# Kernel tuning notes

Hardware: AMD Instinct MI355X
Metric: run time of the kernel (lower is better)

## Reference

```python
import jax, jax.numpy as jnp
import numpy as np

N = 50000        # nodes
E = 800000       # edges (avg degree 16)
IN = 256         # in_feature_dim
H = 4            # heads_num
F = 64           # out_feature_dim per head (H*F == IN)
NEG_SLOPE = 0.2  # LeakyReLU slope used for both scoring and output activation


def setup_inputs() -> dict:
    key = jax.random.key(0)
    ks = jax.random.split(key, 8)
    x = jax.random.normal(ks[0], (N, IN), dtype=jnp.float32)
    edge_src = jax.random.randint(ks[1], (E,), 0, N, dtype=jnp.int32)
    edge_trg = jax.random.randint(ks[2], (E,), 0, N, dtype=jnp.int32)
    # xavier-ish scaled params
    W = jax.random.normal(ks[3], (IN, H * F), dtype=jnp.float32) * 0.06
    a_src = jax.random.normal(ks[4], (H, F), dtype=jnp.float32) * 0.1
    a_trg = jax.random.normal(ks[5], (H, F), dtype=jnp.float32) * 0.1
    skip_w = jax.random.normal(ks[6], (IN, H * F), dtype=jnp.float32) * 0.06
    bias = jnp.zeros((H * F,), dtype=jnp.float32)
    return {"x": x, "W": W, "a_src": a_src, "a_trg": a_trg,
            "skip_w": skip_w, "bias": bias,
            "edge_src": edge_src, "edge_trg": edge_trg}


def _leaky(v):
    return jnp.where(v > 0, v, NEG_SLOPE * v)


def reference(x, W, a_src, a_trg, skip_w, bias, edge_src, edge_trg):
    n_nodes = x.shape[0]
    # node-wise projection: [N, H, F]
    proj = (x @ W).reshape(n_nodes, H, F)
    # per-head attention scores: [N, H]
    s_src = jnp.einsum('nhf,hf->nh', proj, a_src)
    s_trg = jnp.einsum('nhf,hf->nh', proj, a_trg)
    # lift to edges + LeakyReLU scoring: [E, H]
    e = _leaky(s_src[edge_src] + s_trg[edge_trg])
    # neighborhood-aware (scatter) softmax over incoming edges of each target
    e = e - jnp.max(e)                      # global max subtraction, as in the source
    ex = jnp.exp(e)
    denom = jax.ops.segment_sum(ex, edge_trg, num_segments=n_nodes)  # [N, H]
    attn = ex / (denom[edge_trg] + 1e-16)   # [E, H]
    # weighted aggregation: [E, H, F] -> scatter-add -> [N, H, F]
    weighted = proj[edge_src] * attn[..., None]
    out = jax.ops.segment_sum(weighted, edge_trg, num_segments=n_nodes)
    # skip connection (dims differ: in=256 vs per-head 64 -> use skip_proj)
    out = out + (x @ skip_w).reshape(n_nodes, H, F)
    # concat heads + bias + output activation (default LeakyReLU 0.2)
    out = out.reshape(n_nodes, H * F) + bias
    return _leaky(out)
```

## Files before the change

### kernel.cpp

```cpp
#include <hip/hip_runtime.h>
#include <math.h>

constexpr float SLOPE = 0.2f;

typedef __bf16 bf16x8 __attribute__((ext_vector_type(8)));
typedef __bf16 bf16x4 __attribute__((ext_vector_type(4)));
typedef float  f32x4  __attribute__((ext_vector_type(4)));

__device__ __forceinline__ int imin(int a, int b) { return a < b ? a : b; }

__device__ __forceinline__ void glds16(const void* g, void* l) {
    __builtin_amdgcn_global_load_lds(
        (const __attribute__((address_space(1))) unsigned int*)g,
        (__attribute__((address_space(3))) unsigned int*)l,
        16, 0, 0);
}

__global__ __launch_bounds__(256) void prep_k(
    const float* __restrict__ W, const float* __restrict__ skw,
    __bf16* __restrict__ Bt,
    const float* __restrict__ x, __bf16* __restrict__ xb, int nxv, int nxb,
    const int* __restrict__ etrg, int* __restrict__ cnt, int E)
{
    const int b = blockIdx.x;
    if (b < 512) {
        const int i = b * 256 + threadIdx.x;
        const int n = i >> 8, k = i & 255;
        const float v = (n < 256) ? W[k * 256 + n] : skw[k * 256 + (n - 256)];
        Bt[i] = (__bf16)v;
    } else if (b < 512 + nxb) {
        const int gid = (b - 512) * 256 + threadIdx.x;
        if (gid < nxv) {
            const float4 f0 = *(const float4*)(x + (size_t)gid * 8);
            const float4 f1 = *(const float4*)(x + (size_t)gid * 8 + 4);
            bf16x8 v;
            v[0] = (__bf16)f0.x; v[1] = (__bf16)f0.y;
            v[2] = (__bf16)f0.z; v[3] = (__bf16)f0.w;
            v[4] = (__bf16)f1.x; v[5] = (__bf16)f1.y;
            v[6] = (__bf16)f1.z; v[7] = (__bf16)f1.w;
            *(bf16x8*)(xb + (size_t)gid * 8) = v;
        }
    } else {
        const int e = (b - 512 - nxb) * 256 + threadIdx.x;
        if (e < E) atomicAdd(&cnt[etrg[e]], 1);
    }
}

__global__ __launch_bounds__(256) void gemm_mfma(
    const __bf16* __restrict__ xb, const __bf16* __restrict__ Bt,
    __bf16* __restrict__ projb, float* __restrict__ out, int M)
{
    __shared__ __bf16 As[128 * 32];
    __shared__ __bf16 Bs[128 * 32];

    const int t    = threadIdx.x;
    const int w    = t >> 6;
    const int lane = t & 63;
    const int q    = lane >> 4;
    const int ln   = lane & 15;

    const int row0 = blockIdx.x * 128;
    const int bt0  = blockIdx.y * 128;

    f32x4 acc[2][8] = {};

    for (int k0 = 0; k0 < 256; k0 += 32) {
#pragma unroll
        for (int p = 0; p < 2; ++p) {
            const int idx = p * 256 + t;
            const int r   = idx >> 2;
            const int ko  = (idx & 3) * 8;
            const int ga  = imin(row0 + r, M - 1);
            glds16(xb + (size_t)ga * 256 + k0 + ko, &As[idx * 8]);
            glds16(Bt + (size_t)(bt0 + r) * 256 + k0 + ko, &Bs[idx * 8]);
        }
        asm volatile("s_waitcnt vmcnt(0)" ::: "memory");
        __syncthreads();

        bf16x8 af[2], bfr[8];
#pragma unroll
        for (int rb = 0; rb < 2; ++rb)
            af[rb] = *(const bf16x8*)&As[(w * 32 + rb * 16 + ln) * 32 + q * 8];
#pragma unroll
        for (int cb = 0; cb < 8; ++cb)
            bfr[cb] = *(const bf16x8*)&Bs[(cb * 16 + ln) * 32 + q * 8];
#pragma unroll
        for (int rb = 0; rb < 2; ++rb)
#pragma unroll
            for (int cb = 0; cb < 8; ++cb)
                acc[rb][cb] = __builtin_amdgcn_mfma_f32_16x16x32_bf16(
                    af[rb], bfr[cb], acc[rb][cb], 0, 0, 0);
        __syncthreads();
    }

    const bool isProj  = (blockIdx.y < 2);
    const int  colbase = (blockIdx.y & 1) * 128;
#pragma unroll
    for (int rb = 0; rb < 2; ++rb) {
#pragma unroll
        for (int r = 0; r < 4; ++r) {
            const int grow = row0 + w * 32 + rb * 16 + q * 4 + r;
            if (grow < M) {
#pragma unroll
                for (int cb = 0; cb < 8; ++cb) {
                    const float v = acc[rb][cb][r];
                    const int gcol = colbase + cb * 16 + ln;
                    if (isProj) projb[(size_t)grow * 256 + gcol] = (__bf16)v;
                    else        out[(size_t)grow * 256 + gcol]   = v;
                }
            }
        }
    }
}

__global__ __launch_bounds__(256) void scores_k(
    const __bf16* __restrict__ projb,
    const float* __restrict__ a_src, const float* __restrict__ a_trg,
    float* __restrict__ s_src, float* __restrict__ s_trg, int N)
{
    const int nid  = blockIdx.x * 4 + (threadIdx.x >> 6);
    const int lane = threadIdx.x & 63;
    if (nid >= N) return;

    const bf16x4 p4  = *(const bf16x4*)(projb + (size_t)nid * 256 + lane * 4);
    const float4 as4 = *(const float4*)(a_src + lane * 4);
    const float4 at4 = *(const float4*)(a_trg + lane * 4);

    float vs = (float)p4[0] * as4.x + (float)p4[1] * as4.y +
               (float)p4[2] * as4.z + (float)p4[3] * as4.w;
    float vt = (float)p4[0] * at4.x + (float)p4[1] * at4.y +
               (float)p4[2] * at4.z + (float)p4[3] * at4.w;

#pragma unroll
    for (int d = 8; d > 0; d >>= 1) {
        vs += __shfl_down(vs, d, 16);
        vt += __shfl_down(vt, d, 16);
    }
    if ((lane & 15) == 0) {
        s_src[nid * 4 + (lane >> 4)] = vs;
        s_trg[nid * 4 + (lane >> 4)] = vt;
    }
}

__global__ __launch_bounds__(1024) void scanA(
    const int* __restrict__ cnt, int* __restrict__ off, int* __restrict__ bsum, int N)
{
    __shared__ int wsum[16];
    const int t = threadIdx.x;
    const int lane = t & 63;
    const int w = t >> 6;
    const int i = blockIdx.x * 1024 + t;
    const int v = (i < N) ? cnt[i] : 0;

    int s = v;
#pragma unroll
    for (int d = 1; d < 64; d <<= 1) {
        int o = __shfl_up(s, d);
        if (lane >= d) s += o;
    }
    if (lane == 63) wsum[w] = s;
    __syncthreads();
    if (w == 0 && lane < 16) {
        int ws = wsum[lane];
        int sc = ws;
#pragma unroll
        for (int d = 1; d < 16; d <<= 1) {
            int o = __shfl_up(sc, d);
            if (lane >= d) sc += o;
        }
        wsum[lane] = sc - ws;
    }
    __syncthreads();
    const int excl = wsum[w] + s - v;
    if (i < N) off[i] = excl;
    if (t == 1023) bsum[blockIdx.x] = excl + v;
}

__global__ __launch_bounds__(256) void scanBC(
    int* __restrict__ off, const int* __restrict__ bsum, int* __restrict__ cur,
    int N, int E)
{
    const int i = blockIdx.x * 256 + threadIdx.x;
    const int chunk = blockIdx.x >> 2;
    const int lane = threadIdx.x & 63;

    int v = (lane < chunk) ? bsum[lane] : 0;
#pragma unroll
    for (int d = 1; d < 64; d <<= 1) v += __shfl_xor(v, d);

    if (i < N) {
        const int o = off[i] + v;
        off[i] = o;
        cur[i] = o;
    }
    if (i == 0) off[N] = E;
}

__global__ __launch_bounds__(256) void scatter_k(
    const int* __restrict__ esrc, const int* __restrict__ etrg,
    int* __restrict__ cur,
    const float* __restrict__ s_src, const float* __restrict__ s_trg,
    int* __restrict__ srcs, float* __restrict__ exs, int E)
{
    const int e = blockIdx.x * 256 + threadIdx.x;
    if (e >= E) return;
    const int s  = esrc[e];
    const int tg = etrg[e];
    const int pos = atomicAdd(&cur[tg], 1);
    srcs[pos] = s;
    const float4 ss = *(const float4*)(s_src + (size_t)s * 4);
    const float4 st = *(const float4*)(s_trg + (size_t)tg * 4);
    float4 ex; float v;
    v = ss.x + st.x; v = v > 0.f ? v : SLOPE * v; ex.x = __expf(v);
    v = ss.y + st.y; v = v > 0.f ? v : SLOPE * v; ex.y = __expf(v);
    v = ss.z + st.z; v = v > 0.f ? v : SLOPE * v; ex.z = __expf(v);
    v = ss.w + st.w; v = v > 0.f ? v : SLOPE * v; ex.w = __expf(v);
    *(float4*)(exs + (size_t)pos * 4) = ex;
}

__global__ __launch_bounds__(256) void aggregate_csr(
    const int* __restrict__ off, const int* __restrict__ srcs,
    const float* __restrict__ exs, const __bf16* __restrict__ projb,
    const float* __restrict__ bias, float* __restrict__ out)
{
    const int n = blockIdx.x;
    const int t = threadIdx.x;
    const int h = t >> 6;

    const int b0 = off[n], b1 = off[n + 1];

    float acc = 0.f, denom = 0.f;
    int i = b0;
    for (; i + 8 <= b1; i += 8) {
        int s[8];
#pragma unroll
        for (int j = 0; j < 8; ++j) s[j] = srcs[i + j];
        float p[8];
#pragma unroll
        for (int j = 0; j < 8; ++j)
            p[j] = (float)projb[(unsigned)s[j] * 256u + t];
        const float* ep = exs + (size_t)i * 4 + h;
        float e[8];
#pragma unroll
        for (int j = 0; j < 8; ++j) e[j] = ep[j * 4];
#pragma unroll
        for (int j = 0; j < 8; ++j) { denom += e[j]; acc += e[j] * p[j]; }
    }
    for (; i < b1; ++i) {
        const int s = srcs[i];
        const float e = exs[(size_t)i * 4 + h];
        denom += e;
        acc += e * (float)projb[(unsigned)s * 256u + t];
    }

    const size_t o = (size_t)n * 256 + t;
    float val = acc / (denom + 1e-16f) + out[o] + bias[t];
    out[o] = val > 0.f ? val : SLOPE * val;
}

extern "C" void kernel_launch(void* const* d_in, const int* in_sizes, int n_in,
                              void* d_out, int out_size, void* d_ws, size_t ws_size,
                              hipStream_t stream)
{
    const float* x     = (const float*)d_in[0];
    const float* W     = (const float*)d_in[1];
    const float* a_src = (const float*)d_in[2];
    const float* a_trg = (const float*)d_in[3];
    const float* skw   = (const float*)d_in[4];
    const float* bias  = (const float*)d_in[5];
    const int*   esrc  = (const int*)d_in[6];
    const int*   etrg  = (const int*)d_in[7];

    const int N = in_sizes[0] / 256;
    const int E = in_sizes[6];
    float* out = (float*)d_out;

    __bf16* projb = (__bf16*)d_ws;
    __bf16* Bt    = projb + (size_t)N * 256;
    __bf16* xb    = Bt + 512 * 256;
    float*  exs   = (float*)xb;
    float*  s_src = (float*)(xb + (size_t)N * 256);
    float*  s_trg = s_src + (size_t)N * 4;
    int*    cnt   = (int*)(s_trg + (size_t)N * 4);
    int*    off   = cnt + N;
    int*    cur   = off + (N + 1);
    int*    bsum  = cur + N;
    int*    srcs  = bsum + 64;

    const int nxv = (N * 256) / 8;
    const int nxb = (nxv + 255) / 256;
    const int nhb = (E + 255) / 256;
    const int nsc = (N + 1023) / 1024;

    hipMemsetAsync(cnt, 0, (size_t)N * sizeof(int), stream);

    prep_k<<<512 + nxb + nhb, 256, 0, stream>>>(W, skw, Bt, x, xb, nxv, nxb,
                                                etrg, cnt, E);

    dim3 g((N + 127) / 128, 4);
    gemm_mfma<<<g, 256, 0, stream>>>(xb, Bt, projb, out, N);

    scores_k<<<(N + 3) / 4, 256, 0, stream>>>(projb, a_src, a_trg, s_src, s_trg, N);

    scanA<<<nsc, 1024, 0, stream>>>(cnt, off, bsum, N);
    scanBC<<<(N + 255) / 256, 256, 0, stream>>>(off, bsum, cur, N, E);

    scatter_k<<<(E + 255) / 256, 256, 0, stream>>>(esrc, etrg, cur, s_src, s_trg,
                                                   srcs, exs, E);

    aggregate_csr<<<N, 256, 0, stream>>>(off, srcs, exs, projb, bias, out);
}
```

Before: 340.6 us.

## Fuse edge scoring into wave-per-node aggregation and enlarge GEMM row tile

Edge score computation (LeakyReLU plus exp) moves from the scatter kernel into a new aggregation kernel. That kernel assigns one 64-lane wave per target node, with each lane handling 4 features via bf16x4 loads, and lanes share source indices and exp values through shuffles. This drops the exs write/read round trip and raises per-lane work in aggregation. Separately, the GEMM tile grows to 256 rows with a launch_bounds occupancy hint, which raises register pressure and lowers block count.

```diff
diff --git a/kernel.cpp b/kernel.cpp
--- a/kernel.cpp
+++ b/kernel.cpp
@@ -46,11 +46,11 @@
     }
 }
 
-__global__ __launch_bounds__(256) void gemm_mfma(
+__global__ __launch_bounds__(256, 2) void gemm_mfma(
     const __bf16* __restrict__ xb, const __bf16* __restrict__ Bt,
     __bf16* __restrict__ projb, float* __restrict__ out, int M)
 {
-    __shared__ __bf16 As[128 * 32];
+    __shared__ __bf16 As[256 * 32];
     __shared__ __bf16 Bs[128 * 32];
 
     const int t    = threadIdx.x;
@@ -59,33 +59,39 @@
     const int q    = lane >> 4;
     const int ln   = lane & 15;
 
-    const int row0 = blockIdx.x * 128;
+    const int row0 = blockIdx.x * 256;
     const int bt0  = blockIdx.y * 128;
 
-    f32x4 acc[2][8] = {};
+    f32x4 acc[4][8] = {};
 
     for (int k0 = 0; k0 < 256; k0 += 32) {
 #pragma unroll
-        for (int p = 0; p < 2; ++p) {
+        for (int p = 0; p < 4; ++p) {
             const int idx = p * 256 + t;
             const int r   = idx >> 2;
             const int ko  = (idx & 3) * 8;
             const int ga  = imin(row0 + r, M - 1);
             glds16(xb + (size_t)ga * 256 + k0 + ko, &As[idx * 8]);
+        }
+#pragma unroll
+        for (int p = 0; p < 2; ++p) {
+            const int idx = p * 256 + t;
+            const int r   = idx >> 2;
+            const int ko  = (idx & 3) * 8;
             glds16(Bt + (size_t)(bt0 + r) * 256 + k0 + ko, &Bs[idx * 8]);
         }
         asm volatile("s_waitcnt vmcnt(0)" ::: "memory");
         __syncthreads();
 
-        bf16x8 af[2], bfr[8];
-#pragma unroll
-        for (int rb = 0; rb < 2; ++rb)
-            af[rb] = *(const bf16x8*)&As[(w * 32 + rb * 16 + ln) * 32 + q * 8];
+        bf16x8 af[4], bfr[8];
+#pragma unroll
+        for (int rb = 0; rb < 4; ++rb)
+            af[rb] = *(const bf16x8*)&As[(w * 64 + rb * 16 + ln) * 32 + q * 8];
 #pragma unroll
         for (int cb = 0; cb < 8; ++cb)
             bfr[cb] = *(const bf16x8*)&Bs[(cb * 16 + ln) * 32 + q * 8];
 #pragma unroll
-        for (int rb = 0; rb < 2; ++rb)
+        for (int rb = 0; rb < 4; ++rb)
 #pragma unroll
             for (int cb = 0; cb < 8; ++cb)
                 acc[rb][cb] = __builtin_amdgcn_mfma_f32_16x16x32_bf16(
@@ -96,10 +102,10 @@
     const bool isProj  = (blockIdx.y < 2);
     const int  colbase = (blockIdx.y & 1) * 128;
 #pragma unroll
-    for (int rb = 0; rb < 2; ++rb) {
+    for (int rb = 0; rb < 4; ++rb) {
 #pragma unroll
         for (int r = 0; r < 4; ++r) {
-            const int grow = row0 + w * 32 + rb * 16 + q * 4 + r;
+            const int grow = row0 + w * 64 + rb * 16 + q * 4 + r;
             if (grow < M) {
 #pragma unroll
                 for (int cb = 0; cb < 8; ++cb) {
@@ -198,64 +204,90 @@
 
 __global__ __launch_bounds__(256) void scatter_k(
     const int* __restrict__ esrc, const int* __restrict__ etrg,
-    int* __restrict__ cur,
+    int* __restrict__ cur, int* __restrict__ srcs, int E)
+{
+    const int e = blockIdx.x * 256 + threadIdx.x;
+    if (e < E) {
+        const int pos = atomicAdd(&cur[etrg[e]], 1);
+        srcs[pos] = esrc[e];
+    }
+}
+
+__global__ __launch_bounds__(256) void aggregate_wave(
+    const int* __restrict__ off, const int* __restrict__ srcs,
     const float* __restrict__ s_src, const float* __restrict__ s_trg,
-    int* __restrict__ srcs, float* __restrict__ exs, int E)
-{
-    const int e = blockIdx.x * 256 + threadIdx.x;
-    if (e >= E) return;
-    const int s  = esrc[e];
-    const int tg = etrg[e];
-    const int pos = atomicAdd(&cur[tg], 1);
-    srcs[pos] = s;
-    const float4 ss = *(const float4*)(s_src + (size_t)s * 4);
-    const float4 st = *(const float4*)(s_trg + (size_t)tg * 4);
-    float4 ex; float v;
-    v = ss.x + st.x; v = v > 0.f ? v : SLOPE * v; ex.x = __expf(v);
-    v = ss.y + st.y; v = v > 0.f ? v : SLOPE * v; ex.y = __expf(v);
-    v = ss.z + st.z; v = v > 0.f ? v : SLOPE * v; ex.z = __expf(v);
-    v = ss.w + st.w; v = v > 0.f ? v : SLOPE * v; ex.w = __expf(v);
-    *(float4*)(exs + (size_t)pos * 4) = ex;
-}
-
-__global__ __launch_bounds__(256) void aggregate_csr(
-    const int* __restrict__ off, const int* __restrict__ srcs,
-    const float* __restrict__ exs, const __bf16* __restrict__ projb,
-    const float* __restrict__ bias, float* __restrict__ out)
-{
-    const int n = blockIdx.x;
-    const int t = threadIdx.x;
-    const int h = t >> 6;
-
+    const __bf16* __restrict__ projb, const float* __restrict__ bias,
+    float* __restrict__ out, int N)
+{
+    const int w = threadIdx.x >> 6;
+    const int l = threadIdx.x & 63;
+    const int n = blockIdx.x * 4 + w;
+    if (n >= N) return;
+
+    const int h  = l >> 4;
+    const int je = l & 7;
+    const float st = s_trg[n * 4 + h];
     const int b0 = off[n], b1 = off[n + 1];
 
-    float acc = 0.f, denom = 0.f;
+    f32x4 acc = {0.f, 0.f, 0.f, 0.f};
+    float denom = 0.f;
+
     int i = b0;
     for (; i + 8 <= b1; i += 8) {
+        const int s0 = srcs[i + je];
+        float v = s_src[s0 * 4 + h] + st;
+        v = v > 0.f ? v : SLOPE * v;
+        const float ex = __expf(v);
+
         int s[8];
 #pragma unroll
-        for (int j = 0; j < 8; ++j) s[j] = srcs[i + j];
-        float p[8];
+        for (int j = 0; j < 8; ++j) s[j] = __shfl(s0, j);
+
+        bf16x4 p[8];
 #pragma unroll
         for (int j = 0; j < 8; ++j)
-            p[j] = (float)projb[(unsigned)s[j] * 256u + t];
-        const float* ep = exs + (size_t)i * 4 + h;
+            p[j] = *(const bf16x4*)(projb + (size_t)((unsigned)s[j] * 256u) + l * 4);
+
         float e[8];
 #pragma unroll
-        for (int j = 0; j < 8; ++j) e[j] = ep[j * 4];
-#pragma unroll
-        for (int j = 0; j < 8; ++j) { denom += e[j]; acc += e[j] * p[j]; }
+        for (int j = 0; j < 8; ++j) e[j] = __shfl(ex, (l & 48) | j);
+
+#pragma unroll
+        for (int j = 0; j < 8; ++j) {
+            denom += e[j];
+            acc[0] += e[j] * (float)p[j][0];
+            acc[1] += e[j] * (float)p[j][1];
+            acc[2] += e[j] * (float)p[j][2];
+            acc[3] += e[j] * (float)p[j][3];
+        }
     }
     for (; i < b1; ++i) {
         const int s = srcs[i];
-        const float e = exs[(size_t)i * 4 + h];
-        denom += e;
-        acc += e * (float)projb[(unsigned)s * 256u + t];
-    }
-
-    const size_t o = (size_t)n * 256 + t;
-    float val = acc / (denom + 1e-16f) + out[o] + bias[t];
-    out[o] = val > 0.f ? val : SLOPE * val;
+        float v = s_src[s * 4 + h] + st;
+        v = v > 0.f ? v : SLOPE * v;
+        const float ex = __expf(v);
+        denom += ex;
+        const bf16x4 p = *(const bf16x4*)(projb + (size_t)((unsigned)s * 256u) + l * 4);
+        acc[0] += ex * (float)p[0];
+        acc[1] += ex * (float)p[1];
+        acc[2] += ex * (float)p[2];
+        acc[3] += ex * (float)p[3];
+    }
+
+    const size_t o = (size_t)n * 256 + l * 4;
+    const float4 sk = *(const float4*)(out + o);
+    const float4 b4 = *(const float4*)(bias + l * 4);
+    const float inv = 1.f / (denom + 1e-16f);
+    float4 r;
+    r.x = acc[0] * inv + sk.x + b4.x;
+    r.y = acc[1] * inv + sk.y + b4.y;
+    r.z = acc[2] * inv + sk.z + b4.z;
+    r.w = acc[3] * inv + sk.w + b4.w;
+    r.x = r.x > 0.f ? r.x : SLOPE * r.x;
+    r.y = r.y > 0.f ? r.y : SLOPE * r.y;
+    r.z = r.z > 0.f ? r.z : SLOPE * r.z;
+    r.w = r.w > 0.f ? r.w : SLOPE * r.w;
+    *(float4*)(out + o) = r;
 }
 
 extern "C" void kernel_launch(void* const* d_in, const int* in_sizes, int n_in,
@@ -278,7 +310,6 @@
     __bf16* projb = (__bf16*)d_ws;
     __bf16* Bt    = projb + (size_t)N * 256;
     __bf16* xb    = Bt + 512 * 256;
-    float*  exs   = (float*)xb;
     float*  s_src = (float*)(xb + (size_t)N * 256);
     float*  s_trg = s_src + (size_t)N * 4;
     int*    cnt   = (int*)(s_trg + (size_t)N * 4);
@@ -297,7 +328,7 @@
     prep_k<<<512 + nxb + nhb, 256, 0, stream>>>(W, skw, Bt, x, xb, nxv, nxb,
                                                 etrg, cnt, E);
 
-    dim3 g((N + 127) / 128, 4);
+    dim3 g((N + 255) / 256, 4);
     gemm_mfma<<<g, 256, 0, stream>>>(xb, Bt, projb, out, N);
 
     scores_k<<<(N + 3) / 4, 256, 0, stream>>>(projb, a_src, a_trg, s_src, s_trg, N);
@@ -305,8 +336,8 @@
     scanA<<<nsc, 1024, 0, stream>>>(cnt, off, bsum, N);
     scanBC<<<(N + 255) / 256, 256, 0, stream>>>(off, bsum, cur, N, E);
 
-    scatter_k<<<(E + 255) / 256, 256, 0, stream>>>(esrc, etrg, cur, s_src, s_trg,
-                                                   srcs, exs, E);
-
-    aggregate_csr<<<N, 256, 0, stream>>>(off, srcs, exs, projb, bias, out);
-}
+    scatter_k<<<(E + 255) / 256, 256, 0, stream>>>(esrc, etrg, cur, srcs, E);
+
+    aggregate_wave<<<(N + 3) / 4, 256, 0, stream>>>(off, srcs, s_src, s_trg,
+                                                    projb, bias, out, N);
+}
```

After: 309.5 us. 9.1% less time.
